# Optimization experiments

Measured on AMD Instinct MI355X. Metric: run time of the kernel, lower is better.

## Reference

```python
import jax, jax.numpy as jnp
import numpy as np

D, H, B = 512, 8, 64
NF, NO = 16384, 8192
EPS = 1e-5


def _ln(x):
    m = jnp.mean(x, axis=-1, keepdims=True)
    v = jnp.mean((x - m) ** 2, axis=-1, keepdims=True)
    return (x - m) / jnp.sqrt(v + EPS)


def setup_inputs() -> dict:
    key = jax.random.key(0)
    ks = jax.random.split(key, 16)
    s = 1.0 / np.sqrt(D)
    inp = {
        "hf": jax.random.normal(ks[0], (NF, D), jnp.float32),
        "ho": jax.random.normal(ks[1], (NO, D), jnp.float32),
        "ps": jax.random.normal(ks[2], (B, D), jnp.float32),
        "face_batch": jnp.sort(jax.random.randint(ks[3], (NF,), 0, B)),
        "obj_batch": jnp.sort(jax.random.randint(ks[4], (NO,), 0, B)),
        "Wq": jax.random.normal(ks[5], (D, D), jnp.float32) * s,
        "bq": jnp.zeros((D,), jnp.float32),
        "Wk": jax.random.normal(ks[6], (D, D), jnp.float32) * s,
        "bk": jnp.zeros((D,), jnp.float32),
        "Wv": jax.random.normal(ks[7], (D, D), jnp.float32) * s,
        "bv": jnp.zeros((D,), jnp.float32),
        "Wo": jax.random.normal(ks[8], (D, D), jnp.float32) * s,
        "bo": jnp.zeros((D,), jnp.float32),
        "Wg": jax.random.normal(ks[9], (D, D), jnp.float32) * s,
        "bg": jnp.full((D,), -1.0, jnp.float32),  # init.constant_(bias, -1.0)
        "alpha": jax.random.normal(ks[10], (D,), jnp.float32) * 0.1,
    }
    return inp


def reference(hf, ho, ps, face_batch, obj_batch, Wq, bq, Wk, bk, Wv, bv, Wo, bo, Wg, bg, alpha):
    dh = D // H
    nodes = jnp.concatenate([hf, ho], axis=0)            # (N, D)
    seg = jnp.concatenate([face_batch, obj_batch], 0)    # (N,)
    N = nodes.shape[0]

    # single-query cross-attention done as ragged/segment attention
    # (identical math to padded MHA with key_padding_mask)
    q = (ps @ Wq + bq).reshape(B, H, dh)                 # (B, H, dh)
    k = (nodes @ Wk + bk).reshape(N, H, dh)
    v = (nodes @ Wv + bv).reshape(N, H, dh)

    scores = jnp.einsum("nhd,nhd->nh", k, q[seg]) / np.sqrt(dh)   # (N, H)
    mx = jax.ops.segment_max(scores, seg, num_segments=B)          # (B, H)
    e = jnp.exp(scores - mx[seg])                                  # (N, H)
    denom = jax.ops.segment_sum(e, seg, num_segments=B)            # (B, H)
    num = jax.ops.segment_sum(e[:, :, None] * v, seg, num_segments=B)  # (B, H, dh)
    attn = (num / denom[:, :, None]).reshape(B, D)
    attn_out = attn @ Wo + bo

    fs = _ln(ps + attn_out)                               # (B, D)
    gate = jax.nn.sigmoid(hf @ Wg + bg)                   # (NF, D)
    signal = alpha * fs[face_batch]                       # (NF, D)
    hf_new = _ln(hf + gate * signal)
    return hf_new, fs
```

## Files before the change

### kernel.cpp

```cpp
#include <hip/hip_runtime.h>
#include <hip/hip_bf16.h>
#include <math.h>

constexpr int D  = 512;
constexpr int H  = 8;
constexpr int DH = 64;
constexpr int B  = 64;
constexpr int NF = 16384;
constexpr int NO = 8192;
constexpr int NT = NF + NO;
constexpr float EPS = 1e-5f;
constexpr float LOG2E = 1.4426950408889634f;

typedef short short8 __attribute__((ext_vector_type(8)));
typedef float f32x4 __attribute__((ext_vector_type(4)));
typedef unsigned short ushort;
typedef ushort ushort8v __attribute__((ext_vector_type(8)));

__device__ __forceinline__ ushort f2bf(float f) {
  unsigned int x = __float_as_uint(f);
  x += 0x7FFF + ((x >> 16) & 1);
  return (ushort)(x >> 16);
}
__device__ __forceinline__ float bf2f(ushort u) {
  return __uint_as_float(((unsigned int)u) << 16);
}
__device__ __forceinline__ float fast_exp(float x) {
  return __builtin_amdgcn_exp2f(x * LOG2E);
}
__device__ __forceinline__ float fast_sigmoid(float z) {
  return __builtin_amdgcn_rcpf(1.0f + __builtin_amdgcn_exp2f(-z * LOG2E));
}
__device__ __forceinline__ short8 cvt8(float4 f0, float4 f1) {
  union { short8 v; __hip_bfloat162 h[4]; } u;
  u.h[0] = __float22bfloat162_rn(float2{f0.x, f0.y});
  u.h[1] = __float22bfloat162_rn(float2{f0.z, f0.w});
  u.h[2] = __float22bfloat162_rn(float2{f1.x, f1.y});
  u.h[3] = __float22bfloat162_rn(float2{f1.z, f1.w});
  return u.v;
}
__device__ __forceinline__ void gll16(const void* g, void* l) {
  __builtin_amdgcn_global_load_lds(
      (const __attribute__((address_space(1))) void*)g,
      (__attribute__((address_space(3))) void*)l, 16, 0, 0);
}

__global__ __launch_bounds__(256) void k_qproj(const float* __restrict__ ps,
                                               const float* __restrict__ Wq,
                                               const float* __restrict__ bq,
                                               float* __restrict__ q) {
  __shared__ float row[D];
  int b = blockIdx.x, cg = blockIdx.y, t = threadIdx.x;
  for (int i = t; i < D; i += 256) row[i] = ps[(size_t)b * D + i];
  __syncthreads();
  int col = cg * 64 + (t >> 2), eq = t & 3;
  float acc = 0.f;
  const float* wp = Wq + (size_t)(eq * 128) * D + col;
  #pragma unroll 8
  for (int e = 0; e < 128; ++e) acc += row[eq * 128 + e] * wp[(size_t)e * D];
  acc += __shfl_xor(acc, 1); acc += __shfl_xor(acc, 2);
  if (eq == 0) q[(size_t)b * D + col] = acc + bq[col];
}

__global__ __launch_bounds__(256) void k_pkproj(const float* __restrict__ q,
                                                const float* __restrict__ Wk,
                                                const float* __restrict__ bk,
                                                float* __restrict__ Pk,
                                                float* __restrict__ qbk) {
  int b = blockIdx.x, h = blockIdx.y;
  __shared__ float qs[DH];
  __shared__ float bks[DH];
  int t = threadIdx.x;
  if (t < DH) { qs[t] = q[b * D + h * DH + t]; bks[t] = bk[h * DH + t]; }
  __syncthreads();
  for (int e = t; e < D; e += 256) {
    float acc = 0.f;
    #pragma unroll 8
    for (int j = 0; j < DH; ++j) acc += Wk[(size_t)e * D + h * DH + j] * qs[j];
    Pk[((size_t)b * H + h) * D + e] = acc;
  }
  if (t == 0) {
    float s = 0.f;
    for (int j = 0; j < DH; ++j) s += bks[j] * qs[j];
    qbk[b * H + h] = s;
  }
}

__global__ void k_bounds(const int* __restrict__ fb, const int* __restrict__ ob,
                         int* __restrict__ fstart, int* __restrict__ ostart) {
  int t = threadIdx.x;
  if (t <= B) {
    int lo = 0, hi = NF;
    while (lo < hi) { int mid = (lo + hi) >> 1; if (fb[mid] < t) lo = mid + 1; else hi = mid; }
    fstart[t] = lo;
  } else if (t >= 128 && t <= 128 + B) {
    int v = t - 128;
    int lo = 0, hi = NO;
    while (lo < hi) { int mid = (lo + hi) >> 1; if (ob[mid] < v) lo = mid + 1; else hi = mid; }
    ostart[v] = lo;
  }
}

__global__ __launch_bounds__(256) void k_scores(const float* __restrict__ hf,
                                                const float* __restrict__ ho,
                                                const int* __restrict__ fb,
                                                const int* __restrict__ ob,
                                                const float* __restrict__ Pk,
                                                const float* __restrict__ qbk,
                                                float* __restrict__ scores) {
  int lane = threadIdx.x & 63;
  int n = blockIdx.x * 4 + (threadIdx.x >> 6);
  int b; const float* row;
  if (n < NF) { b = fb[n]; row = hf + (size_t)n * D; }
  else        { b = ob[n - NF]; row = ho + (size_t)(n - NF) * D; }
  const float4* r4 = (const float4*)row;
  float4 x0 = r4[lane * 2], x1 = r4[lane * 2 + 1];
  float acc[H];
  #pragma unroll
  for (int h = 0; h < H; ++h) {
    const float4* p4 = (const float4*)(Pk + ((size_t)b * H + h) * D) + lane * 2;
    float4 p0 = p4[0], p1 = p4[1];
    acc[h] = x0.x * p0.x + x0.y * p0.y + x0.z * p0.z + x0.w * p0.w +
             x1.x * p1.x + x1.y * p1.y + x1.z * p1.z + x1.w * p1.w;
  }
  #pragma unroll
  for (int h = 0; h < H; ++h) {
    float v = acc[h];
    #pragma unroll
    for (int off = 32; off; off >>= 1) v += __shfl_xor(v, off);
    if (lane == h) scores[(size_t)n * H + h] = (v + qbk[b * H + h]) * 0.125f;
  }
}

__global__ __launch_bounds__(512) void k_segsoftmax(const float* __restrict__ scores,
                                                    const int* __restrict__ fstart,
                                                    const int* __restrict__ ostart,
                                                    float* __restrict__ evals,
                                                    float* __restrict__ denom) {
  int b = blockIdx.x;
  int h = threadIdx.x >> 6, lane = threadIdx.x & 63;
  int f0 = fstart[b], f1 = fstart[b + 1];
  int o0 = ostart[b], o1 = ostart[b + 1];
  float m = -1e30f;
  for (int i = f0 + lane; i < f1; i += 64) m = fmaxf(m, scores[(size_t)i * H + h]);
  for (int i = o0 + lane; i < o1; i += 64) m = fmaxf(m, scores[(size_t)(NF + i) * H + h]);
  #pragma unroll
  for (int off = 32; off; off >>= 1) m = fmaxf(m, __shfl_xor(m, off));
  float s = 0.f;
  for (int i = f0 + lane; i < f1; i += 64) {
    float e = fast_exp(scores[(size_t)i * H + h] - m);
    evals[(size_t)i * H + h] = e; s += e;
  }
  for (int i = o0 + lane; i < o1; i += 64) {
    float e = fast_exp(scores[(size_t)(NF + i) * H + h] - m);
    evals[(size_t)(NF + i) * H + h] = e; s += e;
  }
  #pragma unroll
  for (int off = 32; off; off >>= 1) s += __shfl_xor(s, off);
  if (lane == 0) denom[b * H + h] = s;
}

__global__ __launch_bounds__(512) void k_Taccum(const float* __restrict__ hf,
                                                const float* __restrict__ ho,
                                                const int* __restrict__ fstart,
                                                const int* __restrict__ ostart,
                                                const float* __restrict__ evals,
                                                float* __restrict__ T8) {
  int b = blockIdx.x, chunk = blockIdx.y;
  int e = threadIdx.x;
  int f0 = fstart[b], flen = fstart[b + 1] - f0;
  int o0 = ostart[b], olen = ostart[b + 1] - o0;
  int L = flen + olen;
  float acc[8] = {0.f, 0.f, 0.f, 0.f, 0.f, 0.f, 0.f, 0.f};
  for (int idx = chunk; idx < L; idx += 8) {
    int n; const float* row;
    if (idx < flen) { n = f0 + idx; row = hf + (size_t)n * D; }
    else            { n = NF + o0 + (idx - flen); row = ho + (size_t)(o0 + idx - flen) * D; }
    float x = row[e];
    const float4* ev = (const float4*)(evals + (size_t)n * H);
    float4 e0 = ev[0], e1 = ev[1];
    acc[0] += e0.x * x; acc[1] += e0.y * x; acc[2] += e0.z * x; acc[3] += e0.w * x;
    acc[4] += e1.x * x; acc[5] += e1.y * x; acc[6] += e1.z * x; acc[7] += e1.w * x;
  }
  #pragma unroll
  for (int h = 0; h < H; ++h)
    T8[(((size_t)chunk * B + b) * H + h) * D + e] = acc[h];
}

__global__ __launch_bounds__(256) void k_attn(const float* __restrict__ T8,
                                              const float* __restrict__ denom,
                                              const float* __restrict__ Wv,
                                              const float* __restrict__ bv,
                                              float* __restrict__ attn) {
  __shared__ float Ts[D];
  int b = blockIdx.x, h = blockIdx.y, t = threadIdx.x;
  for (int i = t; i < D; i += 256) {
    float s = 0.f;
    #pragma unroll
    for (int c2 = 0; c2 < 8; ++c2)
      s += T8[(((size_t)c2 * B + b) * H + h) * D + i];
    Ts[i] = s;
  }
  __syncthreads();
  int col = h * DH + (t >> 2), eq = t & 3;
  float acc = 0.f;
  const float* wp = Wv + (size_t)(eq * 128) * D + col;
  #pragma unroll 8
  for (int e = 0; e < 128; ++e) acc += Ts[eq * 128 + e] * wp[(size_t)e * D];
  acc += __shfl_xor(acc, 1); acc += __shfl_xor(acc, 2);
  if (eq == 0) attn[(size_t)b * D + col] = acc / denom[b * H + h] + bv[col];
}

__global__ __launch_bounds__(256) void k_x(const float* __restrict__ attn,
                                           const float* __restrict__ Wo,
                                           const float* __restrict__ bo,
                                           const float* __restrict__ ps,
                                           float* __restrict__ x) {
  __shared__ float As[D];
  int b = blockIdx.x, cg = blockIdx.y, t = threadIdx.x;
  for (int i = t; i < D; i += 256) As[i] = attn[(size_t)b * D + i];
  __syncthreads();
  int col = cg * 64 + (t >> 2), eq = t & 3;
  float acc = 0.f;
  const float* wp = Wo + (size_t)(eq * 128) * D + col;
  #pragma unroll 8
  for (int e = 0; e < 128; ++e) acc += As[eq * 128 + e] * wp[(size_t)e * D];
  acc += __shfl_xor(acc, 1); acc += __shfl_xor(acc, 2);
  if (eq == 0) x[(size_t)b * D + col] = acc + bo[col] + ps[(size_t)b * D + col];
}

__global__ __launch_bounds__(512) void k_ln(const float* __restrict__ x,
                                            float* __restrict__ fs) {
  __shared__ float redS[8], redQ[8];
  __shared__ float sM, sI;
  int b = blockIdx.x, t = threadIdx.x;
  float v = x[(size_t)b * D + t];
  float s = v, sq = v * v;
  #pragma unroll
  for (int off = 32; off; off >>= 1) { s += __shfl_xor(s, off); sq += __shfl_xor(sq, off); }
  int wv = t >> 6, ln = t & 63;
  if (ln == 0) { redS[wv] = s; redQ[wv] = sq; }
  __syncthreads();
  if (t == 0) {
    float S = 0.f, Q = 0.f;
    #pragma unroll
    for (int i = 0; i < 8; ++i) { S += redS[i]; Q += redQ[i]; }
    float mean = S * (1.f / D);
    float var = Q * (1.f / D) - mean * mean;
    sM = mean; sI = rsqrtf(var + EPS);
  }
  __syncthreads();
  fs[(size_t)b * D + t] = (v - sM) * sI;
}

__global__ __launch_bounds__(256) void k_prepW(const float* __restrict__ Wg,
                                               ushort* __restrict__ Wgt) {
  __shared__ float tile[32][33];
  int bx = blockIdx.x, by = blockIdx.y;
  int tx = threadIdx.x & 31, ty = threadIdx.x >> 5;
  #pragma unroll
  for (int i = 0; i < 4; ++i)
    tile[ty + i * 8][tx] = Wg[(size_t)(by * 32 + ty + i * 8) * D + bx * 32 + tx];
  __syncthreads();
  #pragma unroll
  for (int i = 0; i < 4; ++i)
    Wgt[(size_t)(bx * 32 + ty + i * 8) * D + by * 32 + tx] = f2bf(tile[tx][ty + i * 8]);
}

__global__ __launch_bounds__(256) void k_gate(const float* __restrict__ hf,
                                              const ushort* __restrict__ Wgt,
                                              const float* __restrict__ bg,
                                              ushort* __restrict__ gateb) {
  __shared__ float  Asf[2][4096];
  __shared__ ushort Bs[2][4096];
  const int tid = threadIdx.x, lane = tid & 63, w = tid >> 6;
  const int rowBase = blockIdx.x * 128, colBase = blockIdx.y * 128;
  const int wm = w >> 1, wn = w & 1;
  const int lrow = lane & 15, kg = lane >> 4;

  int ia[4], ra[4], ca[4];
  #pragma unroll
  for (int j = 0; j < 4; ++j) {
    ia[j] = (w * 4 + j) * 64 + lane;
    ra[j] = ia[j] >> 3;
    ca[j] = (ia[j] & 7) ^ (ra[j] & 7);
  }
  int ib[2], cb[2], cc[2];
  #pragma unroll
  for (int j = 0; j < 2; ++j) {
    ib[j] = (w * 2 + j) * 64 + lane;
    cb[j] = ib[j] >> 2;
    cc[j] = (ib[j] & 3) ^ ((cb[j] >> 1) & 3);
  }

#define STAGE(buf, k0)                                                          \
  {                                                                             \
    _Pragma("unroll")                                                           \
    for (int j = 0; j < 4; ++j)                                                 \
      gll16(hf + (size_t)(rowBase + ra[j]) * D + (k0) + ca[j] * 4,              \
            &Asf[buf][(w * 4 + j) * 256]);                                      \
    _Pragma("unroll")                                                           \
    for (int j = 0; j < 2; ++j)                                                 \
      gll16(Wgt + (size_t)(colBase + cb[j]) * D + (k0) + cc[j] * 8,             \
            &Bs[buf][(w * 2 + j) * 512]);                                       \
  }

  STAGE(0, 0);
  __syncthreads();

  f32x4 acc[4][4] = {};
  for (int t = 0; t < 16; ++t) {
    const int cur = t & 1;
    if (t < 15) STAGE(cur ^ 1, (t + 1) * 32);
    short8 av[4], bv[4];
    #pragma unroll
    for (int m = 0; m < 4; ++m) {
      const int a_r = wm * 64 + m * 16 + lrow;
      const float* Ab = &Asf[cur][a_r * 32];
      const int c0 = (2 * kg) ^ (a_r & 7), c1 = (2 * kg + 1) ^ (a_r & 7);
      av[m] = cvt8(*(const float4*)(Ab + c0 * 4), *(const float4*)(Ab + c1 * 4));
    }
    #pragma unroll
    for (int n = 0; n < 4; ++n) {
      const int b_c = wn * 64 + n * 16 + lrow;
      bv[n] = *(const short8*)&Bs[cur][b_c * 32 + (kg ^ ((b_c >> 1) & 3)) * 8];
    }
    #pragma unroll
    for (int m = 0; m < 4; ++m)
      #pragma unroll
      for (int n = 0; n < 4; ++n)
        acc[m][n] = __builtin_amdgcn_mfma_f32_16x16x32_bf16(av[m], bv[n], acc[m][n], 0, 0, 0);
    __syncthreads();
  }
#undef STAGE

  #pragma unroll
  for (int n = 0; n < 4; ++n) {
    const int col = colBase + wn * 64 + n * 16 + lrow;
    const float bgv = bg[col];
    #pragma unroll
    for (int m = 0; m < 4; ++m) {
      const int row0 = rowBase + wm * 64 + m * 16 + kg * 4;
      #pragma unroll
      for (int r = 0; r < 4; ++r)
        gateb[(size_t)(row0 + r) * D + col] = f2bf(fast_sigmoid(acc[m][n][r] + bgv));
    }
  }
}

__global__ __launch_bounds__(256) void k_final(const float* __restrict__ hf,
                                               const ushort* __restrict__ gateb,
                                               const float* __restrict__ alpha,
                                               const float* __restrict__ fs,
                                               const int* __restrict__ fb,
                                               float* __restrict__ out) {
  const int w = threadIdx.x >> 6, lane = threadIdx.x & 63;
  const int row = blockIdx.x * 4 + w;
  const int b = fb[row];
  const float* hr = hf + (size_t)row * D + lane * 8;
  const ushort* gr = gateb + (size_t)row * D + lane * 8;
  const float* fr = fs + (size_t)b * D + lane * 8;
  const float* ar = alpha + lane * 8;
  float4 h0 = *(const float4*)hr, h1 = *(const float4*)(hr + 4);
  union { ushort8v v; ushort u[8]; } ug;
  ug.v = *(const ushort8v*)gr;
  float4 p0 = *(const float4*)fr, p1 = *(const float4*)(fr + 4);
  float4 a0 = *(const float4*)ar, a1 = *(const float4*)(ar + 4);
  float hv[8] = {h0.x, h0.y, h0.z, h0.w, h1.x, h1.y, h1.z, h1.w};
  float pv[8] = {p0.x, p0.y, p0.z, p0.w, p1.x, p1.y, p1.z, p1.w};
  float av[8] = {a0.x, a0.y, a0.z, a0.w, a1.x, a1.y, a1.z, a1.w};
  float x[8], s = 0.f, sq = 0.f;
  #pragma unroll
  for (int i = 0; i < 8; ++i) {
    x[i] = hv[i] + bf2f(ug.u[i]) * (av[i] * pv[i]);
    s += x[i]; sq += x[i] * x[i];
  }
  #pragma unroll
  for (int off = 32; off; off >>= 1) { s += __shfl_xor(s, off); sq += __shfl_xor(sq, off); }
  float mean = s * (1.f / D);
  float inv = rsqrtf(sq * (1.f / D) - mean * mean + EPS);
  float* op = out + (size_t)row * D + lane * 8;
  float4 o0 = {(x[0] - mean) * inv, (x[1] - mean) * inv, (x[2] - mean) * inv, (x[3] - mean) * inv};
  float4 o1 = {(x[4] - mean) * inv, (x[5] - mean) * inv, (x[6] - mean) * inv, (x[7] - mean) * inv};
  *(float4*)op = o0;
  *(float4*)(op + 4) = o1;
}

extern "C" void kernel_launch(void* const* d_in, const int* in_sizes, int n_in,
                              void* d_out, int out_size, void* d_ws, size_t ws_size,
                              hipStream_t stream) {
  const float* hf    = (const float*)d_in[0];
  const float* ho    = (const float*)d_in[1];
  const float* ps    = (const float*)d_in[2];
  const int*   fb    = (const int*)d_in[3];
  const int*   ob    = (const int*)d_in[4];
  const float* Wq    = (const float*)d_in[5];
  const float* bq    = (const float*)d_in[6];
  const float* Wk    = (const float*)d_in[7];
  const float* bk    = (const float*)d_in[8];
  const float* Wv    = (const float*)d_in[9];
  const float* bv    = (const float*)d_in[10];
  const float* Wo    = (const float*)d_in[11];
  const float* bo    = (const float*)d_in[12];
  const float* Wg    = (const float*)d_in[13];
  const float* bg    = (const float*)d_in[14];
  const float* alpha = (const float*)d_in[15];

  float* out    = (float*)d_out;
  float* fs_out = out + (size_t)NF * D;

  ushort* Wgt   = (ushort*)d_ws;
  ushort* gateb = Wgt + 512 * 512;
  float* fbase  = (float*)(gateb + (size_t)NF * D);
  float* q      = fbase;
  float* Pk     = q + B * D;
  float* qbk    = Pk + B * H * D;
  float* scores = qbk + B * H;
  float* evals  = scores + (size_t)NT * H;
  float* denom  = evals + (size_t)NT * H;
  float* T8     = denom + B * H;
  float* attn   = T8 + (size_t)8 * B * H * D;
  float* xbuf   = attn + B * D;
  int* fstart   = (int*)(xbuf + B * D);
  int* ostart   = fstart + (B + 1);

  k_prepW<<<dim3(16, 16), 256, 0, stream>>>(Wg, Wgt);
  k_gate<<<dim3(NF / 128, 4), 256, 0, stream>>>(hf, Wgt, bg, gateb);
  k_qproj<<<dim3(B, 8), 256, 0, stream>>>(ps, Wq, bq, q);
  k_pkproj<<<dim3(B, H), 256, 0, stream>>>(q, Wk, bk, Pk, qbk);
  k_bounds<<<1, 256, 0, stream>>>(fb, ob, fstart, ostart);
  k_scores<<<NT / 4, 256, 0, stream>>>(hf, ho, fb, ob, Pk, qbk, scores);
  k_segsoftmax<<<B, 512, 0, stream>>>(scores, fstart, ostart, evals, denom);
  k_Taccum<<<dim3(B, 8), 512, 0, stream>>>(hf, ho, fstart, ostart, evals, T8);
  k_attn<<<dim3(B, H), 256, 0, stream>>>(T8, denom, Wv, bv, attn);
  k_x<<<dim3(B, 8), 256, 0, stream>>>(attn, Wo, bo, ps, xbuf);
  k_ln<<<B, 512, 0, stream>>>(xbuf, fs_out);
  k_final<<<NF / 4, 256, 0, stream>>>(hf, gateb, alpha, fs_out, fb, out);
}
```

Measured before the change: 146.9 us.

## Fuse small prep, gate/scores, and attention-output kernels to cut launches

Merges the q/Pk projections, segment-bounds search and Wg transpose into one heterogeneous prep kernel. It also runs the MFMA gate GEMM and the scores kernel as one launch split by block index, and fuses the Wv, Wo and layernorm tail into one per-batch kernel. This removes kernel launches and inter-kernel gaps and lets the gate GEMM overlap with the score computation. The cost is much less parallelism in the fused tail, since 64 blocks each do two full 512x512 matvecs serially. The combined kernel may also pay extra LDS allocation in its score blocks.

```diff
diff --git a/kernel.cpp b/kernel.cpp
--- a/kernel.cpp
+++ b/kernel.cpp
@@ -12,6 +12,9 @@
 constexpr float EPS = 1e-5f;
 constexpr float LOG2E = 1.4426950408889634f;
 
+constexpr int GATE_BLOCKS = 512;
+constexpr int SCORES_BLOCKS = NT / 4;
+
 typedef short short8 __attribute__((ext_vector_type(8)));
 typedef float f32x4 __attribute__((ext_vector_type(4)));
 typedef unsigned short ushort;
@@ -45,90 +48,192 @@
       (__attribute__((address_space(3))) void*)l, 16, 0, 0);
 }
 
-__global__ __launch_bounds__(256) void k_qproj(const float* __restrict__ ps,
-                                               const float* __restrict__ Wq,
-                                               const float* __restrict__ bq,
-                                               float* __restrict__ q) {
-  __shared__ float row[D];
-  int b = blockIdx.x, cg = blockIdx.y, t = threadIdx.x;
-  for (int i = t; i < D; i += 256) row[i] = ps[(size_t)b * D + i];
+__global__ __launch_bounds__(512) void k_prep_all(const float* __restrict__ ps,
+                                                  const float* __restrict__ Wq,
+                                                  const float* __restrict__ bq,
+                                                  const float* __restrict__ Wk,
+                                                  const float* __restrict__ bk,
+                                                  const float* __restrict__ Wg,
+                                                  const int* __restrict__ fb,
+                                                  const int* __restrict__ ob,
+                                                  float* __restrict__ Pk,
+                                                  float* __restrict__ qbk,
+                                                  ushort* __restrict__ Wgt,
+                                                  int* __restrict__ fstart,
+                                                  int* __restrict__ ostart) {
+  __shared__ float shm[64 * 65];
+  const int bid = blockIdx.x, t = threadIdx.x;
+  if (bid < B) {
+    const int b = bid;
+    if (t < D) shm[t] = ps[(size_t)b * D + t];
+    __syncthreads();
+    {
+      float a0 = bq[t], a1 = 0.f, a2 = 0.f, a3 = 0.f;
+      #pragma unroll 4
+      for (int e = 0; e < D; e += 4) {
+        a0 += shm[e + 0] * Wq[(size_t)(e + 0) * D + t];
+        a1 += shm[e + 1] * Wq[(size_t)(e + 1) * D + t];
+        a2 += shm[e + 2] * Wq[(size_t)(e + 2) * D + t];
+        a3 += shm[e + 3] * Wq[(size_t)(e + 3) * D + t];
+      }
+      shm[512 + t] = a0 + a1 + a2 + a3;
+    }
+    __syncthreads();
+    {
+      const float* wr = Wk + (size_t)t * D;
+      #pragma unroll
+      for (int h = 0; h < H; ++h) {
+        float acc = 0.f;
+        #pragma unroll
+        for (int j4 = 0; j4 < 16; ++j4) {
+          float4 wv = *(const float4*)(wr + h * 64 + j4 * 4);
+          float4 qv = *(const float4*)(&shm[512 + h * 64 + j4 * 4]);
+          acc += wv.x * qv.x + wv.y * qv.y + wv.z * qv.z + wv.w * qv.w;
+        }
+        Pk[((size_t)b * H + h) * D + t] = acc;
+      }
+    }
+    if (t < H) {
+      float s = 0.f;
+      for (int j = 0; j < DH; ++j) s += bk[t * DH + j] * shm[512 + t * DH + j];
+      qbk[b * H + t] = s;
+    }
+  } else if (bid == B) {
+    if (t <= B) {
+      int lo = 0, hi = NF;
+      while (lo < hi) { int mid = (lo + hi) >> 1; if (fb[mid] < t) lo = mid + 1; else hi = mid; }
+      fstart[t] = lo;
+    } else if (t >= 128 && t <= 128 + B) {
+      int v = t - 128;
+      int lo = 0, hi = NO;
+      while (lo < hi) { int mid = (lo + hi) >> 1; if (ob[mid] < v) lo = mid + 1; else hi = mid; }
+      ostart[v] = lo;
+    }
+  } else {
+    const int tb = bid - (B + 1);
+    const int bx = tb & 7, by = tb >> 3;
+    const int tx = t & 63, ty = t >> 6;
+    #pragma unroll
+    for (int i = 0; i < 8; ++i)
+      shm[(ty + 8 * i) * 65 + tx] = Wg[(size_t)(by * 64 + ty + 8 * i) * D + bx * 64 + tx];
+    __syncthreads();
+    #pragma unroll
+    for (int i = 0; i < 8; ++i)
+      Wgt[(size_t)(bx * 64 + ty + 8 * i) * D + by * 64 + tx] = f2bf(shm[tx * 65 + ty + 8 * i]);
+  }
+}
+
+__global__ __launch_bounds__(256) void k_gate_scores(const float* __restrict__ hf,
+                                                     const float* __restrict__ ho,
+                                                     const int* __restrict__ fb,
+                                                     const int* __restrict__ ob,
+                                                     const ushort* __restrict__ Wgt,
+                                                     const float* __restrict__ bg,
+                                                     const float* __restrict__ Pk,
+                                                     const float* __restrict__ qbk,
+                                                     ushort* __restrict__ gateb,
+                                                     float* __restrict__ scores) {
+  __shared__ float  Asf[2][4096];
+  __shared__ ushort Bs[2][4096];
+  const int bid = blockIdx.x;
+  const int tid = threadIdx.x, lane = tid & 63, w = tid >> 6;
+
+  if (bid >= GATE_BLOCKS) {
+    int n = (bid - GATE_BLOCKS) * 4 + w;
+    int b; const float* row;
+    if (n < NF) { b = fb[n]; row = hf + (size_t)n * D; }
+    else        { b = ob[n - NF]; row = ho + (size_t)(n - NF) * D; }
+    const float4* r4 = (const float4*)row;
+    float4 x0 = r4[lane * 2], x1 = r4[lane * 2 + 1];
+    float acc[H];
+    #pragma unroll
+    for (int h = 0; h < H; ++h) {
+      const float4* p4 = (const float4*)(Pk + ((size_t)b * H + h) * D) + lane * 2;
+      float4 p0 = p4[0], p1 = p4[1];
+      acc[h] = x0.x * p0.x + x0.y * p0.y + x0.z * p0.z + x0.w * p0.w +
+               x1.x * p1.x + x1.y * p1.y + x1.z * p1.z + x1.w * p1.w;
+    }
+    #pragma unroll
+    for (int h = 0; h < H; ++h) {
+      float v = acc[h];
+      #pragma unroll
+      for (int off = 32; off; off >>= 1) v += __shfl_xor(v, off);
+      if (lane == h) scores[(size_t)n * H + h] = (v + qbk[b * H + h]) * 0.125f;
+    }
+    return;
+  }
+
+  const int rowBase = (bid & 127) * 128, colBase = (bid >> 7) * 128;
+  const int wm = w >> 1, wn = w & 1;
+  const int lrow = lane & 15, kg = lane >> 4;
+
+  int ra[4], ca[4];
+  #pragma unroll
+  for (int j = 0; j < 4; ++j) {
+    int ia = (w * 4 + j) * 64 + lane;
+    ra[j] = ia >> 3;
+    ca[j] = (ia & 7) ^ (ra[j] & 7);
+  }
+  int cb[2], cc[2];
+  #pragma unroll
+  for (int j = 0; j < 2; ++j) {
+    int ib = (w * 2 + j) * 64 + lane;
+    cb[j] = ib >> 2;
+    cc[j] = (ib & 3) ^ ((cb[j] >> 1) & 3);
+  }
+
+#define STAGE(buf, k0)                                                          \
+  {                                                                             \
+    _Pragma("unroll")                                                           \
+    for (int j = 0; j < 4; ++j)                                                 \
+      gll16(hf + (size_t)(rowBase + ra[j]) * D + (k0) + ca[j] * 4,              \
+            &Asf[buf][(w * 4 + j) * 256]);                                      \
+    _Pragma("unroll")                                                           \
+    for (int j = 0; j < 2; ++j)                                                 \
+      gll16(Wgt + (size_t)(colBase + cb[j]) * D + (k0) + cc[j] * 8,             \
+            &Bs[buf][(w * 2 + j) * 512]);                                       \
+  }
+
+  STAGE(0, 0);
   __syncthreads();
-  int col = cg * 64 + (t >> 2), eq = t & 3;
-  float acc = 0.f;
-  const float* wp = Wq + (size_t)(eq * 128) * D + col;
-  #pragma unroll 8
-  for (int e = 0; e < 128; ++e) acc += row[eq * 128 + e] * wp[(size_t)e * D];
-  acc += __shfl_xor(acc, 1); acc += __shfl_xor(acc, 2);
-  if (eq == 0) q[(size_t)b * D + col] = acc + bq[col];
-}
-
-__global__ __launch_bounds__(256) void k_pkproj(const float* __restrict__ q,
-                                                const float* __restrict__ Wk,
-                                                const float* __restrict__ bk,
-                                                float* __restrict__ Pk,
-                                                float* __restrict__ qbk) {
-  int b = blockIdx.x, h = blockIdx.y;
-  __shared__ float qs[DH];
-  __shared__ float bks[DH];
-  int t = threadIdx.x;
-  if (t < DH) { qs[t] = q[b * D + h * DH + t]; bks[t] = bk[h * DH + t]; }
-  __syncthreads();
-  for (int e = t; e < D; e += 256) {
-    float acc = 0.f;
-    #pragma unroll 8
-    for (int j = 0; j < DH; ++j) acc += Wk[(size_t)e * D + h * DH + j] * qs[j];
-    Pk[((size_t)b * H + h) * D + e] = acc;
-  }
-  if (t == 0) {
-    float s = 0.f;
-    for (int j = 0; j < DH; ++j) s += bks[j] * qs[j];
-    qbk[b * H + h] = s;
-  }
-}
-
-__global__ void k_bounds(const int* __restrict__ fb, const int* __restrict__ ob,
-                         int* __restrict__ fstart, int* __restrict__ ostart) {
-  int t = threadIdx.x;
-  if (t <= B) {
-    int lo = 0, hi = NF;
-    while (lo < hi) { int mid = (lo + hi) >> 1; if (fb[mid] < t) lo = mid + 1; else hi = mid; }
-    fstart[t] = lo;
-  } else if (t >= 128 && t <= 128 + B) {
-    int v = t - 128;
-    int lo = 0, hi = NO;
-    while (lo < hi) { int mid = (lo + hi) >> 1; if (ob[mid] < v) lo = mid + 1; else hi = mid; }
-    ostart[v] = lo;
-  }
-}
-
-__global__ __launch_bounds__(256) void k_scores(const float* __restrict__ hf,
-                                                const float* __restrict__ ho,
-                                                const int* __restrict__ fb,
-                                                const int* __restrict__ ob,
-                                                const float* __restrict__ Pk,
-                                                const float* __restrict__ qbk,
-                                                float* __restrict__ scores) {
-  int lane = threadIdx.x & 63;
-  int n = blockIdx.x * 4 + (threadIdx.x >> 6);
-  int b; const float* row;
-  if (n < NF) { b = fb[n]; row = hf + (size_t)n * D; }
-  else        { b = ob[n - NF]; row = ho + (size_t)(n - NF) * D; }
-  const float4* r4 = (const float4*)row;
-  float4 x0 = r4[lane * 2], x1 = r4[lane * 2 + 1];
-  float acc[H];
-  #pragma unroll
-  for (int h = 0; h < H; ++h) {
-    const float4* p4 = (const float4*)(Pk + ((size_t)b * H + h) * D) + lane * 2;
-    float4 p0 = p4[0], p1 = p4[1];
-    acc[h] = x0.x * p0.x + x0.y * p0.y + x0.z * p0.z + x0.w * p0.w +
-             x1.x * p1.x + x1.y * p1.y + x1.z * p1.z + x1.w * p1.w;
-  }
-  #pragma unroll
-  for (int h = 0; h < H; ++h) {
-    float v = acc[h];
-    #pragma unroll
-    for (int off = 32; off; off >>= 1) v += __shfl_xor(v, off);
-    if (lane == h) scores[(size_t)n * H + h] = (v + qbk[b * H + h]) * 0.125f;
+
+  f32x4 acc[4][4] = {};
+  for (int t = 0; t < 16; ++t) {
+    const int cur = t & 1;
+    if (t < 15) STAGE(cur ^ 1, (t + 1) * 32);
+    short8 av[4], bv[4];
+    #pragma unroll
+    for (int m = 0; m < 4; ++m) {
+      const int a_r = wm * 64 + m * 16 + lrow;
+      const float* Ab = &Asf[cur][a_r * 32];
+      const int c0 = (2 * kg) ^ (a_r & 7), c1 = (2 * kg + 1) ^ (a_r & 7);
+      av[m] = cvt8(*(const float4*)(Ab + c0 * 4), *(const float4*)(Ab + c1 * 4));
+    }
+    #pragma unroll
+    for (int n = 0; n < 4; ++n) {
+      const int b_c = wn * 64 + n * 16 + lrow;
+      bv[n] = *(const short8*)&Bs[cur][b_c * 32 + (kg ^ ((b_c >> 1) & 3)) * 8];
+    }
+    #pragma unroll
+    for (int m = 0; m < 4; ++m)
+      #pragma unroll
+      for (int n = 0; n < 4; ++n)
+        acc[m][n] = __builtin_amdgcn_mfma_f32_16x16x32_bf16(av[m], bv[n], acc[m][n], 0, 0, 0);
+    __syncthreads();
+  }
+#undef STAGE
+
+  #pragma unroll
+  for (int n = 0; n < 4; ++n) {
+    const int col = colBase + wn * 64 + n * 16 + lrow;
+    const float bgv = bg[col];
+    #pragma unroll
+    for (int m = 0; m < 4; ++m) {
+      const int row0 = rowBase + wm * 64 + m * 16 + kg * 4;
+      #pragma unroll
+      for (int r = 0; r < 4; ++r)
+        gateb[(size_t)(row0 + r) * D + col] = f2bf(fast_sigmoid(acc[m][n][r] + bgv));
+    }
   }
 }
 
@@ -187,55 +292,56 @@
     T8[(((size_t)chunk * B + b) * H + h) * D + e] = acc[h];
 }
 
-__global__ __launch_bounds__(256) void k_attn(const float* __restrict__ T8,
-                                              const float* __restrict__ denom,
-                                              const float* __restrict__ Wv,
-                                              const float* __restrict__ bv,
-                                              float* __restrict__ attn) {
-  __shared__ float Ts[D];
-  int b = blockIdx.x, h = blockIdx.y, t = threadIdx.x;
-  for (int i = t; i < D; i += 256) {
-    float s = 0.f;
-    #pragma unroll
-    for (int c2 = 0; c2 < 8; ++c2)
-      s += T8[(((size_t)c2 * B + b) * H + h) * D + i];
-    Ts[i] = s;
-  }
-  __syncthreads();
-  int col = h * DH + (t >> 2), eq = t & 3;
-  float acc = 0.f;
-  const float* wp = Wv + (size_t)(eq * 128) * D + col;
-  #pragma unroll 8
-  for (int e = 0; e < 128; ++e) acc += Ts[eq * 128 + e] * wp[(size_t)e * D];
-  acc += __shfl_xor(acc, 1); acc += __shfl_xor(acc, 2);
-  if (eq == 0) attn[(size_t)b * D + col] = acc / denom[b * H + h] + bv[col];
-}
-
-__global__ __launch_bounds__(256) void k_x(const float* __restrict__ attn,
-                                           const float* __restrict__ Wo,
-                                           const float* __restrict__ bo,
-                                           const float* __restrict__ ps,
-                                           float* __restrict__ x) {
-  __shared__ float As[D];
-  int b = blockIdx.x, cg = blockIdx.y, t = threadIdx.x;
-  for (int i = t; i < D; i += 256) As[i] = attn[(size_t)b * D + i];
-  __syncthreads();
-  int col = cg * 64 + (t >> 2), eq = t & 3;
-  float acc = 0.f;
-  const float* wp = Wo + (size_t)(eq * 128) * D + col;
-  #pragma unroll 8
-  for (int e = 0; e < 128; ++e) acc += As[eq * 128 + e] * wp[(size_t)e * D];
-  acc += __shfl_xor(acc, 1); acc += __shfl_xor(acc, 2);
-  if (eq == 0) x[(size_t)b * D + col] = acc + bo[col] + ps[(size_t)b * D + col];
-}
-
-__global__ __launch_bounds__(512) void k_ln(const float* __restrict__ x,
-                                            float* __restrict__ fs) {
+__global__ __launch_bounds__(512) void k_attn_x_ln(const float* __restrict__ T8,
+                                                   const float* __restrict__ denom,
+                                                   const float* __restrict__ Wv,
+                                                   const float* __restrict__ bv,
+                                                   const float* __restrict__ Wo,
+                                                   const float* __restrict__ bo,
+                                                   const float* __restrict__ ps,
+                                                   float* __restrict__ fs_out) {
+  __shared__ float Ts[H * D];
+  __shared__ float attnS[D];
   __shared__ float redS[8], redQ[8];
   __shared__ float sM, sI;
-  int b = blockIdx.x, t = threadIdx.x;
-  float v = x[(size_t)b * D + t];
-  float s = v, sq = v * v;
+  const int b = blockIdx.x, t = threadIdx.x;
+  #pragma unroll
+  for (int i = 0; i < 8; ++i) {
+    int he = t + i * 512;
+    float s = 0.f;
+    #pragma unroll
+    for (int c2 = 0; c2 < 8; ++c2)
+      s += T8[((size_t)c2 * B + b) * (H * D) + he];
+    Ts[he] = s;
+  }
+  __syncthreads();
+  {
+    const int h = t >> 6;
+    const float* tp = Ts + h * D;
+    float a0 = 0.f, a1 = 0.f, a2 = 0.f, a3 = 0.f;
+    #pragma unroll 4
+    for (int e = 0; e < D; e += 4) {
+      a0 += tp[e + 0] * Wv[(size_t)(e + 0) * D + t];
+      a1 += tp[e + 1] * Wv[(size_t)(e + 1) * D + t];
+      a2 += tp[e + 2] * Wv[(size_t)(e + 2) * D + t];
+      a3 += tp[e + 3] * Wv[(size_t)(e + 3) * D + t];
+    }
+    attnS[t] = (a0 + a1 + a2 + a3) / denom[b * H + h] + bv[t];
+  }
+  __syncthreads();
+  float xv;
+  {
+    float a0 = bo[t] + ps[(size_t)b * D + t], a1 = 0.f, a2 = 0.f, a3 = 0.f;
+    #pragma unroll 4
+    for (int e = 0; e < D; e += 4) {
+      a0 += attnS[e + 0] * Wo[(size_t)(e + 0) * D + t];
+      a1 += attnS[e + 1] * Wo[(size_t)(e + 1) * D + t];
+      a2 += attnS[e + 2] * Wo[(size_t)(e + 2) * D + t];
+      a3 += attnS[e + 3] * Wo[(size_t)(e + 3) * D + t];
+    }
+    xv = a0 + a1 + a2 + a3;
+  }
+  float s = xv, sq = xv * xv;
   #pragma unroll
   for (int off = 32; off; off >>= 1) { s += __shfl_xor(s, off); sq += __shfl_xor(sq, off); }
   int wv = t >> 6, ln = t & 63;
@@ -250,102 +356,7 @@
     sM = mean; sI = rsqrtf(var + EPS);
   }
   __syncthreads();
-  fs[(size_t)b * D + t] = (v - sM) * sI;
-}
-
-__global__ __launch_bounds__(256) void k_prepW(const float* __restrict__ Wg,
-                                               ushort* __restrict__ Wgt) {
-  __shared__ float tile[32][33];
-  int bx = blockIdx.x, by = blockIdx.y;
-  int tx = threadIdx.x & 31, ty = threadIdx.x >> 5;
-  #pragma unroll
-  for (int i = 0; i < 4; ++i)
-    tile[ty + i * 8][tx] = Wg[(size_t)(by * 32 + ty + i * 8) * D + bx * 32 + tx];
-  __syncthreads();
-  #pragma unroll
-  for (int i = 0; i < 4; ++i)
-    Wgt[(size_t)(bx * 32 + ty + i * 8) * D + by * 32 + tx] = f2bf(tile[tx][ty + i * 8]);
-}
-
-__global__ __launch_bounds__(256) void k_gate(const float* __restrict__ hf,
-                                              const ushort* __restrict__ Wgt,
-                                              const float* __restrict__ bg,
-                                              ushort* __restrict__ gateb) {
-  __shared__ float  Asf[2][4096];
-  __shared__ ushort Bs[2][4096];
-  const int tid = threadIdx.x, lane = tid & 63, w = tid >> 6;
-  const int rowBase = blockIdx.x * 128, colBase = blockIdx.y * 128;
-  const int wm = w >> 1, wn = w & 1;
-  const int lrow = lane & 15, kg = lane >> 4;
-
-  int ia[4], ra[4], ca[4];
-  #pragma unroll
-  for (int j = 0; j < 4; ++j) {
-    ia[j] = (w * 4 + j) * 64 + lane;
-    ra[j] = ia[j] >> 3;
-    ca[j] = (ia[j] & 7) ^ (ra[j] & 7);
-  }
-  int ib[2], cb[2], cc[2];
-  #pragma unroll
-  for (int j = 0; j < 2; ++j) {
-    ib[j] = (w * 2 + j) * 64 + lane;
-    cb[j] = ib[j] >> 2;
-    cc[j] = (ib[j] & 3) ^ ((cb[j] >> 1) & 3);
-  }
-
-#define STAGE(buf, k0)                                                          \
-  {                                                                             \
-    _Pragma("unroll")                                                           \
-    for (int j = 0; j < 4; ++j)                                                 \
-      gll16(hf + (size_t)(rowBase + ra[j]) * D + (k0) + ca[j] * 4,              \
-            &Asf[buf][(w * 4 + j) * 256]);                                      \
-    _Pragma("unroll")                                                           \
-    for (int j = 0; j < 2; ++j)                                                 \
-      gll16(Wgt + (size_t)(colBase + cb[j]) * D + (k0) + cc[j] * 8,             \
-            &Bs[buf][(w * 2 + j) * 512]);                                       \
-  }
-
-  STAGE(0, 0);
-  __syncthreads();
-
-  f32x4 acc[4][4] = {};
-  for (int t = 0; t < 16; ++t) {
-    const int cur = t & 1;
-    if (t < 15) STAGE(cur ^ 1, (t + 1) * 32);
-    short8 av[4], bv[4];
-    #pragma unroll
-    for (int m = 0; m < 4; ++m) {
-      const int a_r = wm * 64 + m * 16 + lrow;
-      const float* Ab = &Asf[cur][a_r * 32];
-      const int c0 = (2 * kg) ^ (a_r & 7), c1 = (2 * kg + 1) ^ (a_r & 7);
-      av[m] = cvt8(*(const float4*)(Ab + c0 * 4), *(const float4*)(Ab + c1 * 4));
-    }
-    #pragma unroll
-    for (int n = 0; n < 4; ++n) {
-      const int b_c = wn * 64 + n * 16 + lrow;
-      bv[n] = *(const short8*)&Bs[cur][b_c * 32 + (kg ^ ((b_c >> 1) & 3)) * 8];
-    }
-    #pragma unroll
-    for (int m = 0; m < 4; ++m)
-      #pragma unroll
-      for (int n = 0; n < 4; ++n)
-        acc[m][n] = __builtin_amdgcn_mfma_f32_16x16x32_bf16(av[m], bv[n], acc[m][n], 0, 0, 0);
-    __syncthreads();
-  }
-#undef STAGE
-
-  #pragma unroll
-  for (int n = 0; n < 4; ++n) {
-    const int col = colBase + wn * 64 + n * 16 + lrow;
-    const float bgv = bg[col];
-    #pragma unroll
-    for (int m = 0; m < 4; ++m) {
-      const int row0 = rowBase + wm * 64 + m * 16 + kg * 4;
-      #pragma unroll
-      for (int r = 0; r < 4; ++r)
-        gateb[(size_t)(row0 + r) * D + col] = f2bf(fast_sigmoid(acc[m][n][r] + bgv));
-    }
-  }
+  fs_out[(size_t)b * D + t] = (xv - sM) * sI;
 }
 
 __global__ __launch_bounds__(256) void k_final(const float* __restrict__ hf,
@@ -412,28 +423,21 @@
   ushort* Wgt   = (ushort*)d_ws;
   ushort* gateb = Wgt + 512 * 512;
   float* fbase  = (float*)(gateb + (size_t)NF * D);
-  float* q      = fbase;
-  float* Pk     = q + B * D;
+  float* Pk     = fbase;
   float* qbk    = Pk + B * H * D;
   float* scores = qbk + B * H;
   float* evals  = scores + (size_t)NT * H;
   float* denom  = evals + (size_t)NT * H;
   float* T8     = denom + B * H;
-  float* attn   = T8 + (size_t)8 * B * H * D;
-  float* xbuf   = attn + B * D;
-  int* fstart   = (int*)(xbuf + B * D);
+  int* fstart   = (int*)(T8 + (size_t)8 * B * H * D);
   int* ostart   = fstart + (B + 1);
 
-  k_prepW<<<dim3(16, 16), 256, 0, stream>>>(Wg, Wgt);
-  k_gate<<<dim3(NF / 128, 4), 256, 0, stream>>>(hf, Wgt, bg, gateb);
-  k_qproj<<<dim3(B, 8), 256, 0, stream>>>(ps, Wq, bq, q);
-  k_pkproj<<<dim3(B, H), 256, 0, stream>>>(q, Wk, bk, Pk, qbk);
-  k_bounds<<<1, 256, 0, stream>>>(fb, ob, fstart, ostart);
-  k_scores<<<NT / 4, 256, 0, stream>>>(hf, ho, fb, ob, Pk, qbk, scores);
+  k_prep_all<<<B + 1 + 64, 512, 0, stream>>>(ps, Wq, bq, Wk, bk, Wg, fb, ob,
+                                             Pk, qbk, Wgt, fstart, ostart);
+  k_gate_scores<<<GATE_BLOCKS + SCORES_BLOCKS, 256, 0, stream>>>(
+      hf, ho, fb, ob, Wgt, bg, Pk, qbk, gateb, scores);
   k_segsoftmax<<<B, 512, 0, stream>>>(scores, fstart, ostart, evals, denom);
   k_Taccum<<<dim3(B, 8), 512, 0, stream>>>(hf, ho, fstart, ostart, evals, T8);
-  k_attn<<<dim3(B, H), 256, 0, stream>>>(T8, denom, Wv, bv, attn);
-  k_x<<<dim3(B, 8), 256, 0, stream>>>(attn, Wo, bo, ps, xbuf);
-  k_ln<<<B, 512, 0, stream>>>(xbuf, fs_out);
+  k_attn_x_ln<<<B, 512, 0, stream>>>(T8, denom, Wv, bv, Wo, bo, ps, fs_out);
   k_final<<<NF / 4, 256, 0, stream>>>(hf, gateb, alpha, fs_out, fb, out);
 }
```

After: 186.6 us. +27.0%, slower.
